# Kernel optimization log

Hardware: AMD Instinct MI355X
Metric: run time of the kernel (lower is better)

Reference implementation:

```python
import jax, jax.numpy as jnp
import numpy as np

DIM_U = 36
IDX_E = np.arange(0, 36, 2)   # even nodes (u1)
IDX_O = np.arange(1, 36, 2)   # odd nodes (u2)
# wraparound neighbor index sets (precomputed mod 36, matching torch negative indexing)
IDX_A = np.arange(-1, 34, 2) % 36   # [35,1,3,...,33]
IDX_B = np.arange(1, 36, 2)         # [1,3,...,35]
IDX_C = np.arange(3, 38, 2) % 36    # [3,5,...,35,1]


def setup_inputs() -> dict:
    key = jax.random.key(0)
    ks = jax.random.split(key, 9)
    N, H = 500000, 128
    return {
        "t": 0,
        "u": jax.random.normal(ks[0], (N, DIM_U), dtype=jnp.float32),
        "reg1": jax.random.normal(ks[1], (6,), dtype=jnp.float32),
        "reg2": jax.random.normal(ks[2], (4,), dtype=jnp.float32),
        "W1": jax.random.normal(ks[3], (18, H), dtype=jnp.float32) * 0.1,
        "b1": jax.random.normal(ks[4], (H,), dtype=jnp.float32) * 0.1,
        "W2a": jax.random.normal(ks[5], (H, 18 * 3), dtype=jnp.float32) * 0.1,
        "b2a": jax.random.normal(ks[6], (18 * 3,), dtype=jnp.float32) * 0.1,
        "W2b": jax.random.normal(ks[7], (H, 18 * 4), dtype=jnp.float32) * 0.1,
        "b2b": jax.random.normal(ks[8], (18 * 4,), dtype=jnp.float32) * 0.1,
    }


def _forward(u, reg1, reg2, W1, b1, W2a, b2a, W2b, b2b):
    N = u.shape[0]
    ie = IDX_E
    # features for even nodes: [N, 18, 5]
    x1 = jnp.stack([
        u[:, ie],
        u[:, (ie + 1) % DIM_U],
        u[:, (ie - 2) % DIM_U] * u[:, (ie - 1) % DIM_U],
        u[:, (ie - 1) % DIM_U] * u[:, (ie + 2) % DIM_U],
        u[:, ie] * u[:, (ie + 1) % DIM_U],
    ], axis=-1)
    io = IDX_O
    # features for odd nodes: [N, 18, 3]
    x2 = jnp.stack([
        u[:, io],
        u[:, (io - 2) % DIM_U] * u[:, (io - 1) % DIM_U],
        u[:, (io - 1) % DIM_U] * u[:, (io + 1) % DIM_U],
    ], axis=-1)
    outreg = jnp.zeros_like(u)
    outreg = outreg.at[:, IDX_E].set(jnp.einsum('nij,j->ni', x1, reg1[1:]) + reg1[0])
    outreg = outreg.at[:, IDX_O].set(jnp.einsum('nij,j->ni', x2, reg2[1:]) + reg2[0])
    # --- neural (cgnn) part: MLP 18 -> H -> (18*3, 18*4) ---
    u1 = u[:, IDX_E]                      # [N, 18]
    h = jnp.tanh(u1 @ W1 + b1)            # [N, H]
    out0 = (h @ W2a + b2a).reshape(N, 18, 3)
    out1 = (h @ W2b + b2b).reshape(N, 18, 4)
    uA, uB, uC = u[:, IDX_A], u[:, IDX_B], u[:, IDX_C]
    outnet = jnp.zeros_like(u)
    outnet = outnet.at[:, IDX_E].set(out0[:, :, 0] + out0[:, :, 1] * uA + out0[:, :, 2] * uB)
    outnet = outnet.at[:, IDX_O].set(out1[:, :, 0] + out1[:, :, 1] * uA + out1[:, :, 2] * uB + out1[:, :, 3] * uC)
    return outnet + outreg


def reference(t, u, reg1, reg2, W1, b1, W2a, b2a, W2b, b2b):
    return _forward(u, reg1, reg2, W1, b1, W2a, b2a, W2b, b2b)
```

## Files before the change

kernel.cpp:

```cpp
#include <hip/hip_runtime.h>
#include <cstddef>


typedef __attribute__((ext_vector_type(8))) __bf16 bf16x8;
typedef __attribute__((ext_vector_type(8))) short short8;
typedef __attribute__((ext_vector_type(4))) float f32x4;

__device__ __forceinline__ unsigned short f2bf(float f) {
    unsigned int u = __float_as_uint(f);
    unsigned int r = (u + 0x7FFFu + ((u >> 16) & 1u)) >> 16;
    return (unsigned short)r;
}

__device__ __forceinline__ unsigned int cvt_pk_bf16(float lo, float hi) {
    unsigned int r;
    asm("v_cvt_pk_bf16_f32 %0, %1, %2" : "=v"(r) : "v"(lo), "v"(hi));
    return r;
}

template <typename A>
__device__ __forceinline__ auto mfma_try(A a, A b, f32x4 c, int)
    -> decltype(__builtin_amdgcn_mfma_f32_16x16x32_bf16(a, b, c, 0, 0, 0)) {
    return __builtin_amdgcn_mfma_f32_16x16x32_bf16(a, b, c, 0, 0, 0);
}
template <typename A>
__device__ __forceinline__ f32x4 mfma_try(A a, A b, f32x4 c, long) {
    return __builtin_amdgcn_mfma_f32_16x16x32_bf16(
        __builtin_bit_cast(short8, a), __builtin_bit_cast(short8, b), c, 0, 0, 0);
}
__device__ __forceinline__ f32x4 mfma_bf16(short8 a, short8 b, f32x4 c) {
    return mfma_try(__builtin_bit_cast(bf16x8, a), __builtin_bit_cast(bf16x8, b), c, 0);
}

__device__ __forceinline__ float tanh_pade(float x) {
    const float t = fminf(fmaxf(x, -3.0f), 3.0f);
    const float s = t * t;
    return __fdividef(t * (27.0f + s), fmaf(9.0f, s, 27.0f));
}

__global__ __launch_bounds__(256, 4) void mixmodel_mfma13(
    const float* __restrict__ u,
    const float* __restrict__ reg1,
    const float* __restrict__ reg2,
    const float* __restrict__ W1,
    const float* __restrict__ b1,
    const float* __restrict__ W2a,
    const float* __restrict__ b2a,
    const float* __restrict__ W2b,
    const float* __restrict__ b2b,
    float* __restrict__ out,
    int N, int ntiles)
{
    __shared__ __align__(16) float          u_ext[32 * 40];
    __shared__ __align__(16) unsigned short h_sh[32 * 136];
    __shared__ __align__(16) unsigned short u_bf[32 * 32];
    __shared__ __align__(16) float          c2s[32 * 148];

    const int tid = threadIdx.x;
    const int wid = tid >> 6;
    const int l   = tid & 63;
    const int ln  = l & 15;
    const int lg  = l >> 4;
    const int nb  = wid * 32;

    reinterpret_cast<unsigned int*>(u_bf)[tid]       = 0u;
    reinterpret_cast<unsigned int*>(u_bf)[tid + 256] = 0u;
    __syncthreads();

    short8 b1f[2];
    short8 b2f[2][4];
    f32x4 bias1v[2];
    float bias2[2];
    int c2idx[2];
#pragma unroll
    for (int t = 0; t < 2; ++t) {
        const int n = nb + t * 16 + ln;
        short8 v;
#pragma unroll
        for (int j = 0; j < 8; ++j) {
            const int k = lg * 8 + j;
            const float w = (k < 18) ? W1[k * 128 + n] : 0.0f;
            v[j] = (short)f2bf(w);
        }
        b1f[t] = v;
        bias1v[t] = *reinterpret_cast<const f32x4*>(&b1[nb + t * 16 + lg * 4]);
        bias2[t] = (n < 54) ? b2a[n] : (n < 126 ? b2b[n - 54] : 0.0f);
        if (n < 54)       c2idx[t] = (n / 3) * 8 + (n % 3);
        else if (n < 126) { const int m = n - 54; c2idx[t] = (m >> 2) * 8 + 4 + (m & 3); }
        else              c2idx[t] = 3;
#pragma unroll
        for (int kk = 0; kk < 4; ++kk) {
            short8 w2;
#pragma unroll
            for (int j = 0; j < 8; ++j) {
                const int k = kk * 32 + lg * 8 + j;
                float w;
                if (n < 54)       w = W2a[k * 54 + n];
                else if (n < 126) w = W2b[k * 72 + (n - 54)];
                else              w = 0.0f;
                w2[j] = (short)f2bf(w);
            }
            b2f[t][kk] = w2;
        }
    }

    const float r10 = reg1[0], r11 = reg1[1], r12 = reg1[2];
    const float r13 = reg1[3], r14 = reg1[4], r15 = reg1[5];
    const float r20 = reg2[0], r21 = reg2[1], r22 = reg2[2], r23 = reg2[3];

    const float4* ug = reinterpret_cast<const float4*>(u);
    const long fmax4 = (long)N * 9 - 1;
    const int gs = gridDim.x;

    const int row0 = tid / 9,          c0 = tid - row0 * 9;
    const int row1 = (256 + tid) / 9,  c1 = (256 + tid) - row1 * 9;
    const int hrow = (tid - 192) >> 1, hside = tid & 1;

    float4 pf0, pf1; float2 pfh;
    {
        const int r0 = blockIdx.x * 32;
        long g0 = (long)r0 * 9 + tid; if (g0 > fmax4) g0 = fmax4;
        pf0 = ug[g0];
        if (tid < 32) {
            long g1 = (long)r0 * 9 + 256 + tid; if (g1 > fmax4) g1 = fmax4;
            pf1 = ug[g1];
        }
        if (tid >= 192) {
            int rr = r0 + hrow; if (rr > N - 1) rr = N - 1;
            pfh = *reinterpret_cast<const float2*>(u + (size_t)rr * 36 + (hside ? 0 : 34));
        }
    }

    for (int tile = blockIdx.x; tile < ntiles; tile += gs) {
        {
            float* dst = &u_ext[row0 * 40 + 2 + c0 * 4];
            reinterpret_cast<float2*>(dst)[0] = make_float2(pf0.x, pf0.y);
            reinterpret_cast<float2*>(dst)[1] = make_float2(pf0.z, pf0.w);
            reinterpret_cast<unsigned int*>(u_bf)[row0 * 16 + c0] =
                cvt_pk_bf16(pf0.x, pf0.z);
            if (tid < 32) {
                float* dst1 = &u_ext[row1 * 40 + 2 + c1 * 4];
                reinterpret_cast<float2*>(dst1)[0] = make_float2(pf1.x, pf1.y);
                reinterpret_cast<float2*>(dst1)[1] = make_float2(pf1.z, pf1.w);
                reinterpret_cast<unsigned int*>(u_bf)[row1 * 16 + c1] =
                    cvt_pk_bf16(pf1.x, pf1.z);
            }
            if (tid >= 192)
                *reinterpret_cast<float2*>(&u_ext[hrow * 40 + (hside ? 38 : 0)]) = pfh;

            if (tile + gs < ntiles) {
                const int r0n = (tile + gs) * 32;
                long g0 = (long)r0n * 9 + tid; if (g0 > fmax4) g0 = fmax4;
                pf0 = ug[g0];
                if (tid < 32) {
                    long g1 = (long)r0n * 9 + 256 + tid; if (g1 > fmax4) g1 = fmax4;
                    pf1 = ug[g1];
                }
                if (tid >= 192) {
                    int rr = r0n + hrow; if (rr > N - 1) rr = N - 1;
                    pfh = *reinterpret_cast<const float2*>(u + (size_t)rr * 36 + (hside ? 0 : 34));
                }
            }
        }
        __syncthreads();

#pragma unroll
        for (int rb = 0; rb < 2; ++rb) {
            const short8 a1 = *reinterpret_cast<const short8*>(
                &u_bf[(rb * 16 + ln) * 32 + lg * 8]);
#pragma unroll
            for (int t = 0; t < 2; ++t) {
                const f32x4 h4 = mfma_bf16(b1f[t], a1, bias1v[t]);
                const unsigned int p0 =
                    cvt_pk_bf16(tanh_pade(h4[0]), tanh_pade(h4[1]));
                const unsigned int p1 =
                    cvt_pk_bf16(tanh_pade(h4[2]), tanh_pade(h4[3]));
                *reinterpret_cast<uint2*>(
                    &h_sh[(rb * 16 + ln) * 136 + nb + t * 16 + lg * 4]) =
                    make_uint2(p0, p1);
            }
        }
        __syncthreads();

        f32x4 acc2[2][2];
#pragma unroll
        for (int rb = 0; rb < 2; ++rb)
#pragma unroll
            for (int t = 0; t < 2; ++t) acc2[rb][t] = (f32x4)bias2[t];

#pragma unroll
        for (int rb = 0; rb < 2; ++rb) {
            const int arow = rb * 16 + ln;
#pragma unroll
            for (int kk = 0; kk < 4; ++kk) {
                const short8 a2 = *reinterpret_cast<const short8*>(
                    &h_sh[arow * 136 + kk * 32 + lg * 8]);
#pragma unroll
                for (int t = 0; t < 2; ++t)
                    acc2[rb][t] = mfma_bf16(a2, b2f[t][kk], acc2[rb][t]);
            }
        }

#pragma unroll
        for (int rb = 0; rb < 2; ++rb)
#pragma unroll
            for (int t = 0; t < 2; ++t)
#pragma unroll
                for (int r = 0; r < 4; ++r)
                    c2s[(rb * 16 + lg * 4 + r) * 148 + c2idx[t]] = acc2[rb][t][r];
        __syncthreads();

        const int r0 = tile * 32;
#pragma unroll
        for (int s = 0; s < 3; ++s) {
            const int w = s * 256 + tid;
            if (w < 576) {
                const int row = w / 18;
                const int i   = w - row * 18;
                const int rg  = r0 + row;

                const float2 v0 = *reinterpret_cast<const float2*>(&u_ext[row * 40 + 2 * i]);
                const float2 v1 = *reinterpret_cast<const float2*>(&u_ext[row * 40 + 2 * i + 2]);
                const float2 v2 = *reinterpret_cast<const float2*>(&u_ext[row * 40 + 2 * i + 4]);
                const f32x4  q0 = *reinterpret_cast<const f32x4*>(&c2s[row * 148 + 8 * i]);
                const f32x4  q1 = *reinterpret_cast<const f32x4*>(&c2s[row * 148 + 8 * i + 4]);

                const float um2 = v0.x, uA = v0.y;
                const float ue  = v1.x, uo = v1.y;
                const float up2 = v2.x, uC = v2.y;

                const float oe = q0[0] + q0[1] * uA + q0[2] * uo;
                const float oo = q1[0] + q1[1] * uA + q1[2] * uo + q1[3] * uC;

                float re = r10;
                re = fmaf(r11, ue,       re);
                re = fmaf(r12, uo,       re);
                re = fmaf(r13, um2 * uA, re);
                re = fmaf(r14, uA * up2, re);
                re = fmaf(r15, ue * uo,  re);

                float ro = r20;
                ro = fmaf(r21, uo,       ro);
                ro = fmaf(r22, uA * ue,  ro);
                ro = fmaf(r23, ue * up2, ro);

                if (rg < N)
                    *reinterpret_cast<float2*>(out + (size_t)rg * 36 + 2 * i) =
                        make_float2(oe + re, oo + ro);
            }
        }
        __syncthreads();
    }
}

extern "C" void kernel_launch(void* const* d_in, const int* in_sizes, int n_in,
                              void* d_out, int out_size, void* d_ws, size_t ws_size,
                              hipStream_t stream) {
    const float* u    = (const float*)d_in[1];
    const float* reg1 = (const float*)d_in[2];
    const float* reg2 = (const float*)d_in[3];
    const float* W1   = (const float*)d_in[4];
    const float* b1   = (const float*)d_in[5];
    const float* W2a  = (const float*)d_in[6];
    const float* b2a  = (const float*)d_in[7];
    const float* W2b  = (const float*)d_in[8];
    const float* b2b  = (const float*)d_in[9];
    float* out = (float*)d_out;

    const int N = in_sizes[1] / 36;
    const int ntiles = (N + 31) / 32;
    int grid = ntiles < 1024 ? ntiles : 1024;
    if (grid < 1) grid = 1;
    mixmodel_mfma13<<<grid, 256, 0, stream>>>(u, reg1, reg2, W1, b1,
                                              W2a, b2a, W2b, b2b, out, N, ntiles);
}
```

Before: 75.46 us.

## Use 512-thread blocks with one 16-column MFMA slice per wave

Doubles the block to 512 threads (8 waves), so each wave computes a single 16-wide column slice of the hidden and output layers instead of two. Tile loading, the halo loads and the epilogue loops are remapped to the larger thread count. This cuts per-thread register use and MFMA work per wave, trading it for more waves per block and more idle threads during the load and epilogue phases. Launch bounds move to (512, 8) to raise occupancy.

```diff
diff --git a/kernel.cpp b/kernel.cpp
--- a/kernel.cpp
+++ b/kernel.cpp
@@ -38,7 +38,7 @@
     return __fdividef(t * (27.0f + s), fmaf(9.0f, s, 27.0f));
 }
 
-__global__ __launch_bounds__(256, 4) void mixmodel_mfma13(
+__global__ __launch_bounds__(512, 8) void mixmodel_mfma18(
     const float* __restrict__ u,
     const float* __restrict__ reg1,
     const float* __restrict__ reg2,
@@ -61,20 +61,15 @@
     const int l   = tid & 63;
     const int ln  = l & 15;
     const int lg  = l >> 4;
-    const int nb  = wid * 32;
-
-    reinterpret_cast<unsigned int*>(u_bf)[tid]       = 0u;
-    reinterpret_cast<unsigned int*>(u_bf)[tid + 256] = 0u;
+    const int nb  = wid * 16;
+
+    reinterpret_cast<unsigned int*>(u_bf)[tid] = 0u;
     __syncthreads();
 
-    short8 b1f[2];
-    short8 b2f[2][4];
-    f32x4 bias1v[2];
-    float bias2[2];
-    int c2idx[2];
-#pragma unroll
-    for (int t = 0; t < 2; ++t) {
-        const int n = nb + t * 16 + ln;
+    short8 b1f;
+    f32x4 bias1v;
+    {
+        const int n = nb + ln;
         short8 v;
 #pragma unroll
         for (int j = 0; j < 8; ++j) {
@@ -82,12 +77,19 @@
             const float w = (k < 18) ? W1[k * 128 + n] : 0.0f;
             v[j] = (short)f2bf(w);
         }
-        b1f[t] = v;
-        bias1v[t] = *reinterpret_cast<const f32x4*>(&b1[nb + t * 16 + lg * 4]);
-        bias2[t] = (n < 54) ? b2a[n] : (n < 126 ? b2b[n - 54] : 0.0f);
-        if (n < 54)       c2idx[t] = (n / 3) * 8 + (n % 3);
-        else if (n < 126) { const int m = n - 54; c2idx[t] = (m >> 2) * 8 + 4 + (m & 3); }
-        else              c2idx[t] = 3;
+        b1f = v;
+        bias1v = *reinterpret_cast<const f32x4*>(&b1[nb + lg * 4]);
+    }
+
+    short8 b2f[4];
+    float bias2;
+    int c2idx;
+    {
+        const int n = nb + ln;
+        bias2 = (n < 54) ? b2a[n] : (n < 126 ? b2b[n - 54] : 0.0f);
+        if (n < 54)       c2idx = (n / 3) * 8 + (n % 3);
+        else if (n < 126) { const int m = n - 54; c2idx = (m >> 2) * 8 + 4 + (m & 3); }
+        else              c2idx = 3;
 #pragma unroll
         for (int kk = 0; kk < 4; ++kk) {
             short8 w2;
@@ -100,7 +102,7 @@
                 else              w = 0.0f;
                 w2[j] = (short)f2bf(w);
             }
-            b2f[t][kk] = w2;
+            b2f[kk] = w2;
         }
     }
 
@@ -112,20 +114,17 @@
     const long fmax4 = (long)N * 9 - 1;
     const int gs = gridDim.x;
 
-    const int row0 = tid / 9,          c0 = tid - row0 * 9;
-    const int row1 = (256 + tid) / 9,  c1 = (256 + tid) - row1 * 9;
-    const int hrow = (tid - 192) >> 1, hside = tid & 1;
-
-    float4 pf0, pf1; float2 pfh;
+    const int row0 = tid / 9, c0 = tid - row0 * 9;
+    const int hrow = (tid - 448) >> 1, hside = tid & 1;
+
+    float4 pf0; float2 pfh;
     {
         const int r0 = blockIdx.x * 32;
-        long g0 = (long)r0 * 9 + tid; if (g0 > fmax4) g0 = fmax4;
-        pf0 = ug[g0];
-        if (tid < 32) {
-            long g1 = (long)r0 * 9 + 256 + tid; if (g1 > fmax4) g1 = fmax4;
-            pf1 = ug[g1];
-        }
-        if (tid >= 192) {
+        if (tid < 288) {
+            long g0 = (long)r0 * 9 + tid; if (g0 > fmax4) g0 = fmax4;
+            pf0 = ug[g0];
+        }
+        if (tid >= 448) {
             int rr = r0 + hrow; if (rr > N - 1) rr = N - 1;
             pfh = *reinterpret_cast<const float2*>(u + (size_t)rr * 36 + (hside ? 0 : 34));
         }
@@ -133,30 +132,23 @@
 
     for (int tile = blockIdx.x; tile < ntiles; tile += gs) {
         {
-            float* dst = &u_ext[row0 * 40 + 2 + c0 * 4];
-            reinterpret_cast<float2*>(dst)[0] = make_float2(pf0.x, pf0.y);
-            reinterpret_cast<float2*>(dst)[1] = make_float2(pf0.z, pf0.w);
-            reinterpret_cast<unsigned int*>(u_bf)[row0 * 16 + c0] =
-                cvt_pk_bf16(pf0.x, pf0.z);
-            if (tid < 32) {
-                float* dst1 = &u_ext[row1 * 40 + 2 + c1 * 4];
-                reinterpret_cast<float2*>(dst1)[0] = make_float2(pf1.x, pf1.y);
-                reinterpret_cast<float2*>(dst1)[1] = make_float2(pf1.z, pf1.w);
-                reinterpret_cast<unsigned int*>(u_bf)[row1 * 16 + c1] =
-                    cvt_pk_bf16(pf1.x, pf1.z);
-            }
-            if (tid >= 192)
+            if (tid < 288) {
+                float* dst = &u_ext[row0 * 40 + 2 + c0 * 4];
+                reinterpret_cast<float2*>(dst)[0] = make_float2(pf0.x, pf0.y);
+                reinterpret_cast<float2*>(dst)[1] = make_float2(pf0.z, pf0.w);
+                reinterpret_cast<unsigned int*>(u_bf)[row0 * 16 + c0] =
+                    cvt_pk_bf16(pf0.x, pf0.z);
+            }
+            if (tid >= 448)
                 *reinterpret_cast<float2*>(&u_ext[hrow * 40 + (hside ? 38 : 0)]) = pfh;
 
             if (tile + gs < ntiles) {
                 const int r0n = (tile + gs) * 32;
-                long g0 = (long)r0n * 9 + tid; if (g0 > fmax4) g0 = fmax4;
-                pf0 = ug[g0];
-                if (tid < 32) {
-                    long g1 = (long)r0n * 9 + 256 + tid; if (g1 > fmax4) g1 = fmax4;
-                    pf1 = ug[g1];
+                if (tid < 288) {
+                    long g0 = (long)r0n * 9 + tid; if (g0 > fmax4) g0 = fmax4;
+                    pf0 = ug[g0];
                 }
-                if (tid >= 192) {
+                if (tid >= 448) {
                     int rr = r0n + hrow; if (rr > N - 1) rr = N - 1;
                     pfh = *reinterpret_cast<const float2*>(u + (size_t)rr * 36 + (hside ? 0 : 34));
                 }
@@ -168,25 +160,19 @@
         for (int rb = 0; rb < 2; ++rb) {
             const short8 a1 = *reinterpret_cast<const short8*>(
                 &u_bf[(rb * 16 + ln) * 32 + lg * 8]);
-#pragma unroll
-            for (int t = 0; t < 2; ++t) {
-                const f32x4 h4 = mfma_bf16(b1f[t], a1, bias1v[t]);
-                const unsigned int p0 =
-                    cvt_pk_bf16(tanh_pade(h4[0]), tanh_pade(h4[1]));
-                const unsigned int p1 =
-                    cvt_pk_bf16(tanh_pade(h4[2]), tanh_pade(h4[3]));
-                *reinterpret_cast<uint2*>(
-                    &h_sh[(rb * 16 + ln) * 136 + nb + t * 16 + lg * 4]) =
-                    make_uint2(p0, p1);
-            }
-        }
-        __syncthreads();
-
-        f32x4 acc2[2][2];
-#pragma unroll
-        for (int rb = 0; rb < 2; ++rb)
-#pragma unroll
-            for (int t = 0; t < 2; ++t) acc2[rb][t] = (f32x4)bias2[t];
+            const f32x4 h4 = mfma_bf16(b1f, a1, bias1v);
+            const unsigned int p0 =
+                cvt_pk_bf16(tanh_pade(h4[0]), tanh_pade(h4[1]));
+            const unsigned int p1 =
+                cvt_pk_bf16(tanh_pade(h4[2]), tanh_pade(h4[3]));
+            *reinterpret_cast<uint2*>(
+                &h_sh[(rb * 16 + ln) * 136 + nb + lg * 4]) = make_uint2(p0, p1);
+        }
+        __syncthreads();
+
+        f32x4 acc2[2];
+#pragma unroll
+        for (int rb = 0; rb < 2; ++rb) acc2[rb] = (f32x4)bias2;
 
 #pragma unroll
         for (int rb = 0; rb < 2; ++rb) {
@@ -195,25 +181,21 @@
             for (int kk = 0; kk < 4; ++kk) {
                 const short8 a2 = *reinterpret_cast<const short8*>(
                     &h_sh[arow * 136 + kk * 32 + lg * 8]);
-#pragma unroll
-                for (int t = 0; t < 2; ++t)
-                    acc2[rb][t] = mfma_bf16(a2, b2f[t][kk], acc2[rb][t]);
+                acc2[rb] = mfma_bf16(a2, b2f[kk], acc2[rb]);
             }
         }
 
 #pragma unroll
         for (int rb = 0; rb < 2; ++rb)
 #pragma unroll
-            for (int t = 0; t < 2; ++t)
-#pragma unroll
-                for (int r = 0; r < 4; ++r)
-                    c2s[(rb * 16 + lg * 4 + r) * 148 + c2idx[t]] = acc2[rb][t][r];
+            for (int r = 0; r < 4; ++r)
+                c2s[(rb * 16 + lg * 4 + r) * 148 + c2idx] = acc2[rb][r];
         __syncthreads();
 
         const int r0 = tile * 32;
 #pragma unroll
-        for (int s = 0; s < 3; ++s) {
-            const int w = s * 256 + tid;
+        for (int s = 0; s < 2; ++s) {
+            const int w = s * 512 + tid;
             if (w < 576) {
                 const int row = w / 18;
                 const int i   = w - row * 18;
@@ -271,6 +253,6 @@
     const int ntiles = (N + 31) / 32;
     int grid = ntiles < 1024 ? ntiles : 1024;
     if (grid < 1) grid = 1;
-    mixmodel_mfma13<<<grid, 256, 0, stream>>>(u, reg1, reg2, W1, b1,
+    mixmodel_mfma18<<<grid, 512, 0, stream>>>(u, reg1, reg2, W1, b1,
                                               W2a, b2a, W2b, b2b, out, N, ntiles);
 }
```

After: 97.40 us. 29.1% more time.
